# Kernel tuning notes

Hardware: AMD Instinct MI355X
Metric: run time of the kernel (lower is better)

The kernel has to match this reference:

```python
import jax, jax.numpy as jnp
import numpy as np

D_HEAD = 64
MASK_FILL = -1000000.0


def setup_inputs() -> dict:
    key = jax.random.key(0)
    ks = jax.random.split(key, 5)
    batch, seq, d_model, n_heads, d_head = 4, 2048, 1024, 16, D_HEAD
    # xavier_uniform bound for [d_model, n_heads, d_head]: treated as fan_in=d_model, fan_out=n_heads*d_head
    bound_qkv = float(np.sqrt(6.0 / (d_model + n_heads * d_head)))
    bound_out = float(np.sqrt(6.0 / (d_head + n_heads * d_model)))
    return {
        "resid": jax.random.normal(ks[0], (batch, seq, d_model), dtype=jnp.float32),
        "W_Q": jax.random.uniform(ks[1], (d_model, n_heads, d_head), jnp.float32, -bound_qkv, bound_qkv),
        "W_K": jax.random.uniform(ks[2], (d_model, n_heads, d_head), jnp.float32, -bound_qkv, bound_qkv),
        "W_V": jax.random.uniform(ks[3], (d_model, n_heads, d_head), jnp.float32, -bound_qkv, bound_qkv),
        "W_out": jax.random.uniform(ks[4], (d_head, n_heads, d_model), jnp.float32, -bound_out, bound_out),
        "b_out": jnp.zeros((d_model,), dtype=jnp.float32),
    }


def reference(resid, W_Q, W_K, W_V, W_out, b_out):
    # resid: [b, s, d]; W_Q/K/V: [d, h, dh]; W_out: [dh, h, d]
    seq = resid.shape[1]
    d_head = W_Q.shape[-1]
    q = jnp.einsum('bsd,dhk->bshk', resid, W_Q)
    k = jnp.einsum('bsd,dhk->bshk', resid, W_K)
    v = jnp.einsum('bsd,dhk->bshk', resid, W_V)
    scores = jnp.einsum('bqhk,bkhd->bhqd', q, k.astype(q.dtype)) if False else jnp.einsum('bqhc,bshc->bhqs', q, k)
    scores = scores / jnp.sqrt(jnp.asarray(d_head, dtype=scores.dtype))
    causal_mask = jnp.triu(jnp.ones((seq, seq), dtype=bool), k=1)
    scores = jnp.where(causal_mask, MASK_FILL, scores)
    probs = jax.nn.softmax(scores, axis=-1)  # [b, h, q, s]
    z = jnp.einsum('bhqs,bshc->bqhc', probs, v)
    out = jnp.einsum('bqhc,chd->bqd', z, W_out) + b_out
    return out
```

## Files before the change

kernel.cpp:

```cpp
#include <hip/hip_runtime.h>
#include <hip/hip_bf16.h>


typedef short s16x8 __attribute__((ext_vector_type(8)));
typedef short s16x4 __attribute__((ext_vector_type(4)));
typedef float f32x4 __attribute__((ext_vector_type(4)));

#define MFMA_BF16(A, B, C) __builtin_amdgcn_mfma_f32_16x16x32_bf16((A), (B), (C), 0, 0, 0)

#if __has_builtin(__builtin_amdgcn_exp2f)
#define EXP2(x) __builtin_amdgcn_exp2f(x)
#else
#define EXP2(x) exp2f(x)
#endif
#if __has_builtin(__builtin_amdgcn_rcpf)
#define RCP(x) __builtin_amdgcn_rcpf(x)
#else
#define RCP(x) (1.0f / (x))
#endif

__device__ __forceinline__ short f2bf(float f) {
    __bf16 h = (__bf16)f;
    return __builtin_bit_cast(short, h);
}

__device__ __forceinline__ void gld16(const unsigned short* g, unsigned short* l) {
    __builtin_amdgcn_global_load_lds(
        (const __attribute__((address_space(1))) unsigned int*)g,
        (__attribute__((address_space(3))) unsigned int*)l, 16, 0, 0);
}

__global__ __launch_bounds__(256) void prep_fused(
    const float* __restrict__ resid, const float* __restrict__ WQ,
    const float* __restrict__ WK, const float* __restrict__ WV,
    const float* __restrict__ Wout,
    unsigned short* __restrict__ residb, unsigned short* __restrict__ Wqkvt,
    unsigned short* __restrict__ W2t)
{
    const int bid = blockIdx.x;
    if (bid < 8192) {
        const int i = bid * 256 + threadIdx.x;
        const float4 v = ((const float4*)resid)[i];
        s16x4 o;
        o[0] = f2bf(v.x); o[1] = f2bf(v.y); o[2] = f2bf(v.z); o[3] = f2bf(v.w);
        *(s16x4*)(residb + (size_t)i * 4) = o;
        return;
    }
    __shared__ unsigned short tile[64][66];
    const int id2 = bid - 8192;
    const int which = id2 >> 8;
    const int sub = id2 & 255;
    const int tx = threadIdx.x & 63, ty = threadIdx.x >> 6;
    if (which < 3) {
        const float* W = which == 0 ? WQ : (which == 1 ? WK : WV);
        unsigned short* Wt = Wqkvt + (size_t)which * 1024 * 1024;
        const int n0 = (sub & 15) * 64, k0 = (sub >> 4) * 64;
        #pragma unroll
        for (int i = ty; i < 64; i += 4)
            tile[i][tx] = (unsigned short)f2bf(W[(size_t)(k0 + i) * 1024 + n0 + tx]);
        __syncthreads();
        #pragma unroll
        for (int i = ty; i < 64; i += 4)
            Wt[(size_t)(n0 + i) * 1024 + k0 + tx] = tile[tx][i];
    } else {
        const int d0 = (sub & 15) * 64, h = sub >> 4;
        #pragma unroll
        for (int c = ty; c < 64; c += 4)
            tile[c][tx] = (unsigned short)f2bf(Wout[(size_t)(c * 16 + h) * 1024 + d0 + tx]);
        __syncthreads();
        #pragma unroll
        for (int i = ty; i < 64; i += 4)
            W2t[(size_t)(d0 + i) * 1024 + h * 64 + tx] = tile[tx][i];
    }
}

__global__ __launch_bounds__(512, 2) void gemm_qkv(
    const unsigned short* __restrict__ A,
    const unsigned short* __restrict__ Bt,
    unsigned short* __restrict__ Qb, unsigned short* __restrict__ Kb,
    unsigned short* __restrict__ Vt)
{
    extern __shared__ __align__(16) unsigned short S[];
    constexpr int LDK = 1024, NT = 16;
    const int tid = threadIdx.x, lane = tid & 63, w = tid >> 6;
    const int wm = w >> 2, wn = w & 3;
    const int quad = lane >> 4, fl = lane & 15;

    const int wg  = blockIdx.x;
    const int swz = (wg & 7) * 96 + (wg >> 3);
    const int bx  = swz % 12, by = swz / 12;
    const int m0  = by * 128, n0 = bx * 256;

    const int srow = tid >> 2;
    const int sk   = ((tid & 3) ^ ((tid >> 3) & 3)) * 8;
    const unsigned short* pa  = A  + (size_t)(m0 + srow) * LDK + sk;
    const unsigned short* pb0 = Bt + (size_t)(n0 + srow) * LDK + sk;
    const unsigned short* pb1 = Bt + (size_t)(n0 + 128 + srow) * LDK + sk;
    const int dst = tid * 8;

    const int sx   = (quad ^ ((fl >> 1) & 3)) * 8;
    const int arow = (wm * 64 + fl) * 32 + sx;
    const int brow = 8192 + (wn * 64 + fl) * 32 + sx;

    f32x4 acc[4][4];
    #pragma unroll
    for (int m = 0; m < 4; ++m)
        #pragma unroll
        for (int n = 0; n < 4; ++n) acc[m][n] = (f32x4){0.f, 0.f, 0.f, 0.f};

    gld16(pa,       S + dst);
    gld16(pb0,      S + 8192 + dst);
    gld16(pb1,      S + 12288 + dst);
    gld16(pa + 32,  S + 4096 + dst);
    gld16(pb0 + 32, S + 16384 + dst);
    gld16(pb1 + 32, S + 20480 + dst);

    for (int t = 0; t < NT; ++t) {
        unsigned short* Sc = S + (t & 1) * 24576;
        unsigned short* Sn = S + ((t & 1) ^ 1) * 24576;
        const int ka = (t + 1) * 64;
        const bool pf = (t + 1 < NT);

        asm volatile("s_waitcnt vmcnt(3)" ::: "memory");
        __builtin_amdgcn_s_barrier();

        s16x8 af[4], bfr[4];
        #pragma unroll
        for (int mi = 0; mi < 4; ++mi) af[mi]  = *(const s16x8*)(Sc + arow + mi * 512);
        #pragma unroll
        for (int ni = 0; ni < 4; ++ni) bfr[ni] = *(const s16x8*)(Sc + brow + ni * 512);
        if (pf) {
            gld16(pa + ka,  Sn + dst);
            gld16(pb0 + ka, Sn + 8192 + dst);
            gld16(pb1 + ka, Sn + 12288 + dst);
        }
        asm volatile("" ::: "memory");
        __builtin_amdgcn_s_barrier();
        __builtin_amdgcn_s_setprio(1);
        #pragma unroll
        for (int mi = 0; mi < 4; ++mi)
            #pragma unroll
            for (int ni = 0; ni < 4; ++ni)
                acc[mi][ni] = MFMA_BF16(af[mi], bfr[ni], acc[mi][ni]);
        __builtin_amdgcn_s_setprio(0);

        if (pf) asm volatile("s_waitcnt vmcnt(3)" ::: "memory");
        else    asm volatile("s_waitcnt vmcnt(0)" ::: "memory");
        __builtin_amdgcn_s_barrier();
        #pragma unroll
        for (int mi = 0; mi < 4; ++mi) af[mi]  = *(const s16x8*)(Sc + 4096 + arow + mi * 512);
        #pragma unroll
        for (int ni = 0; ni < 4; ++ni) bfr[ni] = *(const s16x8*)(Sc + 8192 + brow + ni * 512);
        if (pf) {
            gld16(pa + ka + 32,  Sn + 4096 + dst);
            gld16(pb0 + ka + 32, Sn + 16384 + dst);
            gld16(pb1 + ka + 32, Sn + 20480 + dst);
        }
        asm volatile("" ::: "memory");
        __builtin_amdgcn_s_barrier();
        __builtin_amdgcn_s_setprio(1);
        #pragma unroll
        for (int mi = 0; mi < 4; ++mi)
            #pragma unroll
            for (int ni = 0; ni < 4; ++ni)
                acc[mi][ni] = MFMA_BF16(af[mi], bfr[ni], acc[mi][ni]);
        __builtin_amdgcn_s_setprio(0);
    }

    const int which = n0 >> 10;
    if (which < 2) {
        unsigned short* O = which == 0 ? Qb : Kb;
        const int cbase = (n0 & 1023) + wn * 64;
        #pragma unroll
        for (int mi = 0; mi < 4; ++mi) {
            const int row = m0 + wm * 64 + mi * 16 + quad * 4;
            #pragma unroll
            for (int ni = 0; ni < 4; ++ni) {
                const int col = cbase + ni * 16 + fl;
                #pragma unroll
                for (int r = 0; r < 4; ++r)
                    O[(size_t)(row + r) * 1024 + col] = (unsigned short)f2bf(acc[mi][ni][r]);
            }
        }
    } else {
        const int hh = ((n0 - 2048) >> 6) + wn;
        #pragma unroll
        for (int mi = 0; mi < 4; ++mi) {
            const int token = m0 + wm * 64 + mi * 16 + quad * 4;
            const int bb = token >> 11, ss = token & 2047;
            #pragma unroll
            for (int ni = 0; ni < 4; ++ni) {
                const int cl = ni * 16 + fl;
                s16x4 pv;
                pv[0] = f2bf(acc[mi][ni][0]); pv[1] = f2bf(acc[mi][ni][1]);
                pv[2] = f2bf(acc[mi][ni][2]); pv[3] = f2bf(acc[mi][ni][3]);
                *(s16x4*)(Vt + (size_t)((bb * 16 + hh) * 64 + cl) * 2048 + ss) = pv;
            }
        }
    }
}

template <int MODE>
__global__ __launch_bounds__(256, 2) void gemm_bt(
    const unsigned short* __restrict__ A,
    const unsigned short* __restrict__ Bt,
    float* __restrict__ Cf, const float* __restrict__ bias,
    int M, int N, int K)
{
    __shared__ __align__(16) unsigned short AB[2 * 128 * 72];
    const int tid  = threadIdx.x;
    const int lane = tid & 63;
    const int w    = tid >> 6;
    const int wm   = w & 1, wn = w >> 1;
    const int quad = lane >> 4, fl = lane & 15;
    const int m0 = blockIdx.y * 128, n0 = blockIdx.x * 128;

    const unsigned short* gp[9];
    unsigned ldso[9];
    #pragma unroll
    for (int i = 0; i < 9; ++i) {
        const int c = i * 256 + tid;
        const int cm = c % 1152;
        const int r = cm / 9, cl0 = cm % 9;
        const int cl = (cl0 == 8) ? 0 : cl0;
        gp[i] = (c < 1152 ? A + (size_t)(m0 + r) * K : Bt + (size_t)(n0 + r) * K) + cl * 8;
        ldso[i] = (unsigned)c * 8u;
    }

    f32x4 acc[4][4];
    #pragma unroll
    for (int i = 0; i < 4; ++i)
        #pragma unroll
        for (int j = 0; j < 4; ++j)
            acc[i][j] = (f32x4){0.f, 0.f, 0.f, 0.f};

    for (int kt = 0; kt < K; kt += 64) {
        __syncthreads();
        #pragma unroll
        for (int i = 0; i < 9; ++i)
            gld16(gp[i] + kt, AB + ldso[i]);
        __syncthreads();
        #pragma unroll
        for (int ko = 0; ko < 2; ++ko) {
            s16x8 af[4], bf[4];
            #pragma unroll
            for (int mi = 0; mi < 4; ++mi)
                af[mi] = *(const s16x8*)(AB + (wm * 64 + mi * 16 + fl) * 72 + ko * 32 + quad * 8);
            #pragma unroll
            for (int ni = 0; ni < 4; ++ni)
                bf[ni] = *(const s16x8*)(AB + 9216 + (wn * 64 + ni * 16 + fl) * 72 + ko * 32 + quad * 8);
            #pragma unroll
            for (int mi = 0; mi < 4; ++mi)
                #pragma unroll
                for (int ni = 0; ni < 4; ++ni)
                    acc[mi][ni] = MFMA_BF16(af[mi], bf[ni], acc[mi][ni]);
        }
    }

    #pragma unroll
    for (int ni = 0; ni < 4; ++ni) {
        const int col = n0 + wn * 64 + ni * 16 + fl;
        const float bv = bias[col];
        #pragma unroll
        for (int mi = 0; mi < 4; ++mi) {
            const int row = m0 + wm * 64 + mi * 16 + quad * 4;
            #pragma unroll
            for (int r = 0; r < 4; ++r)
                Cf[(size_t)(row + r) * N + col] = acc[mi][ni][r] + bv;
        }
    }
}

template <bool DIAG>
__device__ __forceinline__ void attn_tile(
    int s0, int wl, int wq0, int fl, int quad,
    const unsigned short* __restrict__ KV, const unsigned short* __restrict__ Vs,
    unsigned short* __restrict__ PbW,
    const s16x8 (&qfr)[2][2], f32x4 (&zt)[2][4], float (&ls)[2])
{
    const float SC = 0.18033688011112042f;
    const float M  = 32.0f;
    #pragma unroll
    for (int c4 = 0; c4 < 4; ++c4) {
        if (DIAG && c4 > wl) break;
        #pragma unroll
        for (int e = 0; e < 2; ++e) {
            const int f = 2 * c4 + e;
            const unsigned short* Krow = KV + (f * 16 + fl) * 72;
            const s16x8 kf0 = *(const s16x8*)(Krow + quad * 8);
            const s16x8 kf1 = *(const s16x8*)(Krow + 32 + quad * 8);
            #pragma unroll
            for (int g = 0; g < 2; ++g) {
                unsigned short* pw = PbW + (g * 16 + fl) * 36 + e * 16 + quad * 4;
                if (DIAG && f > 2 * wl + g) {
                    *(s16x4*)pw = (s16x4){0, 0, 0, 0};
                } else {
                    f32x4 z = (f32x4){0.f, 0.f, 0.f, 0.f};
                    z = MFMA_BF16(kf0, qfr[g][0], z);
                    z = MFMA_BF16(kf1, qfr[g][1], z);
                    float p[4];
                    #pragma unroll
                    for (int r = 0; r < 4; ++r) {
                        float arg = fmaf(z[r], SC, -M);
                        if (DIAG && f == 2 * wl + g) {
                            const int s = s0 + f * 16 + quad * 4 + r;
                            const int qi = wq0 + g * 16 + fl;
                            if (s > qi) arg = -100.f;
                        }
                        p[r] = EXP2(arg);
                    }
                    ls[g] += (p[0] + p[1]) + (p[2] + p[3]);
                    s16x4 pk;
                    pk[0] = f2bf(p[0]); pk[1] = f2bf(p[1]);
                    pk[2] = f2bf(p[2]); pk[3] = f2bf(p[3]);
                    *(s16x4*)pw = pk;
                }
            }
        }
        const s16x8 pf0 = *(const s16x8*)(PbW + fl * 36 + quad * 8);
        const s16x8 pf1 = *(const s16x8*)(PbW + (16 + fl) * 36 + quad * 8);
        #pragma unroll
        for (int mf = 0; mf < 4; ++mf) {
            const s16x8 vf = *(const s16x8*)(Vs + (mf * 16 + fl) * 136 + c4 * 32 + quad * 8);
            zt[0][mf] = MFMA_BF16(vf, pf0, zt[0][mf]);
            zt[1][mf] = MFMA_BF16(vf, pf1, zt[1][mf]);
        }
    }
}

__global__ __launch_bounds__(512, 4) void attn_causal(
    const unsigned short* __restrict__ Qb,
    const unsigned short* __restrict__ Kb,
    const unsigned short* __restrict__ Vt,
    unsigned short* __restrict__ Zb)
{
    __shared__ __align__(16) unsigned short KV[17920];
    __shared__ __align__(16) unsigned short Pb[8][32 * 36];
    const int tid = threadIdx.x, lane = tid & 63, w = tid >> 6;
    const int quad = lane >> 4, fl = lane & 15;
    const int lid = blockIdx.x;
    const int g8 = lid >> 6;
    const int qb = g8 < 4 ? 7 - g8 : g8 - 4;
    const int bh = lid & 63, b = bh >> 4, h = bh & 15;
    const int wq0 = qb * 256 + w * 32;
    const int wl = w & 3;
    const int dt = 2 * qb + (w >> 2);

    const unsigned short* Kbase = Kb + (size_t)b * 2048 * 1024 + h * 64;
    const unsigned short* Vbase = Vt + (size_t)bh * 64 * 2048;
    unsigned short* PbW = Pb[w];
    const unsigned short* Vs = KV + 9216;

    s16x8 qfr[2][2];
    #pragma unroll
    for (int g = 0; g < 2; ++g) {
        const unsigned short* Qrow = Qb + (size_t)(b * 2048 + wq0 + g * 16 + fl) * 1024 + h * 64;
        qfr[g][0] = *(const s16x8*)(Qrow + quad * 8);
        qfr[g][1] = *(const s16x8*)(Qrow + 32 + quad * 8);
    }

    const unsigned short* gsp[5];
    int sadv[5];
    unsigned ldsb[5];
    #pragma unroll
    for (int i = 0; i < 5; ++i) {
        const int W = w + 8 * i;
        if (W < 35) {
            const int c = W * 64 + lane;
            if (c < 1152) {
                const int r = c / 9, cl0 = c % 9;
                const int cl = (cl0 == 8) ? 0 : cl0;
                gsp[i] = Kbase + r * 1024 + cl * 8;  sadv[i] = 128 * 1024;
            } else {
                const int cc = c - 1152;
                const int r = cc / 17, cl0 = cc % 17;
                const int cl = (cl0 == 16) ? 0 : cl0;
                gsp[i] = Vbase + r * 2048 + cl * 8;  sadv[i] = 128;
            }
            ldsb[i] = (unsigned)c * 8u;
        }
    }

    f32x4 zt[2][4];
    #pragma unroll
    for (int g = 0; g < 2; ++g)
        #pragma unroll
        for (int mf = 0; mf < 4; ++mf) zt[g][mf] = (f32x4){0.f, 0.f, 0.f, 0.f};
    float ls[2] = {0.f, 0.f};
    const int ntiles = 2 * qb + 2;

    for (int kt = 0; kt < ntiles; ++kt) {
        __syncthreads();
        #pragma unroll
        for (int i = 0; i < 5; ++i)
            if (w + 8 * i < 35)
                gld16(gsp[i], KV + ldsb[i]);
        #pragma unroll
        for (int i = 0; i < 5; ++i)
            if (w + 8 * i < 35)
                gsp[i] += sadv[i];
        __syncthreads();

        if (kt < dt) {
            attn_tile<false>(kt << 7, wl, wq0, fl, quad, KV, Vs, PbW, qfr, zt, ls);
        } else if (kt == dt) {
            attn_tile<true>(kt << 7, wl, wq0, fl, quad, KV, Vs, PbW, qfr, zt, ls);
        }
    }
    #pragma unroll
    for (int g = 0; g < 2; ++g) {
        float lt = ls[g];
        lt += __shfl_xor(lt, 16);
        lt += __shfl_xor(lt, 32);
        const float inv = RCP(lt);
        unsigned short* Zrow = Zb + (size_t)(b * 2048 + wq0 + g * 16 + fl) * 1024 + h * 64;
        #pragma unroll
        for (int mf = 0; mf < 4; ++mf) {
            s16x4 o;
            o[0] = f2bf(zt[g][mf][0] * inv); o[1] = f2bf(zt[g][mf][1] * inv);
            o[2] = f2bf(zt[g][mf][2] * inv); o[3] = f2bf(zt[g][mf][3] * inv);
            *(s16x4*)(Zrow + mf * 16 + quad * 4) = o;
        }
    }
}

extern "C" void kernel_launch(void* const* d_in, const int* in_sizes, int n_in,
                              void* d_out, int out_size, void* d_ws, size_t ws_size,
                              hipStream_t stream) {
    const float* resid = (const float*)d_in[0];
    const float* WQ    = (const float*)d_in[1];
    const float* WK    = (const float*)d_in[2];
    const float* WV    = (const float*)d_in[3];
    const float* Wout  = (const float*)d_in[4];
    const float* bout  = (const float*)d_in[5];
    float* out = (float*)d_out;

    char* p = (char*)d_ws;
    auto alloc = [&](size_t bytes) { void* r = (void*)p; p += (bytes + 255) & ~(size_t)255; return r; };
    unsigned short* residb = (unsigned short*)alloc(8192ull * 1024 * 2);
    unsigned short* Wqkvt  = (unsigned short*)alloc(3072ull * 1024 * 2);
    unsigned short* W2t    = (unsigned short*)alloc(1024ull * 1024 * 2);
    unsigned short* Qbuf   = (unsigned short*)alloc(8192ull * 1024 * 2);
    unsigned short* Kbuf   = (unsigned short*)alloc(8192ull * 1024 * 2);
    unsigned short* Vtb    = (unsigned short*)alloc(64ull * 64 * 2048 * 2);
    unsigned short* Zbuf   = (unsigned short*)alloc(8192ull * 1024 * 2);

    static bool s_attr = false;
    if (!s_attr) {
        hipFuncSetAttribute(reinterpret_cast<const void*>(gemm_qkv),
                            hipFuncAttributeMaxDynamicSharedMemorySize, 98304);
        s_attr = true;
    }

    prep_fused<<<9216, 256, 0, stream>>>(resid, WQ, WK, WV, Wout, residb, Wqkvt, W2t);
    gemm_qkv<<<768, 512, 98304, stream>>>(residb, Wqkvt, Qbuf, Kbuf, Vtb);
    attn_causal<<<512, 512, 0, stream>>>(Qbuf, Kbuf, Vtb, Zbuf);
    gemm_bt<0><<<dim3(8, 64), 256, 0, stream>>>(Zbuf, W2t, out, bout, 8192, 1024, 1024);
}
```

Measured before the change: 263.5 us.

## Deepen QKV GEMM prefetch pipeline and shrink attention blocks to 128 queries

The QKV GEMM now prefetches half-tiles one stage further ahead, so three half-tile loads are in flight (vmcnt 6) instead of one, hiding more global-load latency. The attention kernel goes from 512-thread blocks covering 256 queries to 256-thread blocks covering 128 queries, launching 1024 blocks in longest-first order. Smaller blocks should improve load balance across the causal workload and avoid warps sitting idle on fully masked tiles. The cost is more K/V tile loading per query, since each block loads its own K/V, and more loads issued per thread.

```diff
diff --git a/kernel.cpp b/kernel.cpp
--- a/kernel.cpp
+++ b/kernel.cpp
@@ -114,14 +114,16 @@
     gld16(pa + 32,  S + 4096 + dst);
     gld16(pb0 + 32, S + 16384 + dst);
     gld16(pb1 + 32, S + 20480 + dst);
+    gld16(pa + 64,  S + 24576 + dst);
+    gld16(pb0 + 64, S + 24576 + 8192 + dst);
+    gld16(pb1 + 64, S + 24576 + 12288 + dst);
 
     for (int t = 0; t < NT; ++t) {
         unsigned short* Sc = S + (t & 1) * 24576;
         unsigned short* Sn = S + ((t & 1) ^ 1) * 24576;
-        const int ka = (t + 1) * 64;
-        const bool pf = (t + 1 < NT);
-
-        asm volatile("s_waitcnt vmcnt(3)" ::: "memory");
+
+        if (t < NT - 1) asm volatile("s_waitcnt vmcnt(6)" ::: "memory");
+        else            asm volatile("s_waitcnt vmcnt(3)" ::: "memory");
         __builtin_amdgcn_s_barrier();
 
         s16x8 af[4], bfr[4];
@@ -129,10 +131,11 @@
         for (int mi = 0; mi < 4; ++mi) af[mi]  = *(const s16x8*)(Sc + arow + mi * 512);
         #pragma unroll
         for (int ni = 0; ni < 4; ++ni) bfr[ni] = *(const s16x8*)(Sc + brow + ni * 512);
-        if (pf) {
-            gld16(pa + ka,  Sn + dst);
-            gld16(pb0 + ka, Sn + 8192 + dst);
-            gld16(pb1 + ka, Sn + 12288 + dst);
+        if (t < NT - 1) {
+            const int ka = (t + 1) * 64 + 32;
+            gld16(pa + ka,  Sn + 4096 + dst);
+            gld16(pb0 + ka, Sn + 16384 + dst);
+            gld16(pb1 + ka, Sn + 20480 + dst);
         }
         asm volatile("" ::: "memory");
         __builtin_amdgcn_s_barrier();
@@ -144,17 +147,18 @@
                 acc[mi][ni] = MFMA_BF16(af[mi], bfr[ni], acc[mi][ni]);
         __builtin_amdgcn_s_setprio(0);
 
-        if (pf) asm volatile("s_waitcnt vmcnt(3)" ::: "memory");
-        else    asm volatile("s_waitcnt vmcnt(0)" ::: "memory");
+        if (t < NT - 1) asm volatile("s_waitcnt vmcnt(6)" ::: "memory");
+        else            asm volatile("s_waitcnt vmcnt(0)" ::: "memory");
         __builtin_amdgcn_s_barrier();
         #pragma unroll
         for (int mi = 0; mi < 4; ++mi) af[mi]  = *(const s16x8*)(Sc + 4096 + arow + mi * 512);
         #pragma unroll
         for (int ni = 0; ni < 4; ++ni) bfr[ni] = *(const s16x8*)(Sc + 8192 + brow + ni * 512);
-        if (pf) {
-            gld16(pa + ka + 32,  Sn + 4096 + dst);
-            gld16(pb0 + ka + 32, Sn + 16384 + dst);
-            gld16(pb1 + ka + 32, Sn + 20480 + dst);
+        if (t < NT - 2) {
+            const int ka = (t + 2) * 64;
+            gld16(pa + ka,  Sc + dst);
+            gld16(pb0 + ka, Sc + 8192 + dst);
+            gld16(pb1 + ka, Sc + 12288 + dst);
         }
         asm volatile("" ::: "memory");
         __builtin_amdgcn_s_barrier();
@@ -328,23 +332,21 @@
     }
 }
 
-__global__ __launch_bounds__(512, 4) void attn_causal(
+__global__ __launch_bounds__(256, 3) void attn_causal(
     const unsigned short* __restrict__ Qb,
     const unsigned short* __restrict__ Kb,
     const unsigned short* __restrict__ Vt,
     unsigned short* __restrict__ Zb)
 {
     __shared__ __align__(16) unsigned short KV[17920];
-    __shared__ __align__(16) unsigned short Pb[8][32 * 36];
+    __shared__ __align__(16) unsigned short Pb[4][32 * 36];
     const int tid = threadIdx.x, lane = tid & 63, w = tid >> 6;
     const int quad = lane >> 4, fl = lane & 15;
     const int lid = blockIdx.x;
-    const int g8 = lid >> 6;
-    const int qb = g8 < 4 ? 7 - g8 : g8 - 4;
+    const int qb = 15 - (lid >> 6);
     const int bh = lid & 63, b = bh >> 4, h = bh & 15;
-    const int wq0 = qb * 256 + w * 32;
-    const int wl = w & 3;
-    const int dt = 2 * qb + (w >> 2);
+    const int wq0 = qb * 128 + w * 32;
+    const int wl = w;
 
     const unsigned short* Kbase = Kb + (size_t)b * 2048 * 1024 + h * 64;
     const unsigned short* Vbase = Vt + (size_t)bh * 64 * 2048;
@@ -359,12 +361,12 @@
         qfr[g][1] = *(const s16x8*)(Qrow + 32 + quad * 8);
     }
 
-    const unsigned short* gsp[5];
-    int sadv[5];
-    unsigned ldsb[5];
-    #pragma unroll
-    for (int i = 0; i < 5; ++i) {
-        const int W = w + 8 * i;
+    const unsigned short* gsp[9];
+    int sadv[9];
+    unsigned ldsb[9];
+    #pragma unroll
+    for (int i = 0; i < 9; ++i) {
+        const int W = w + 4 * i;
         if (W < 35) {
             const int c = W * 64 + lane;
             if (c < 1152) {
@@ -387,23 +389,23 @@
         #pragma unroll
         for (int mf = 0; mf < 4; ++mf) zt[g][mf] = (f32x4){0.f, 0.f, 0.f, 0.f};
     float ls[2] = {0.f, 0.f};
-    const int ntiles = 2 * qb + 2;
+    const int ntiles = qb + 1;
 
     for (int kt = 0; kt < ntiles; ++kt) {
         __syncthreads();
         #pragma unroll
-        for (int i = 0; i < 5; ++i)
-            if (w + 8 * i < 35)
+        for (int i = 0; i < 9; ++i)
+            if (w + 4 * i < 35)
                 gld16(gsp[i], KV + ldsb[i]);
         #pragma unroll
-        for (int i = 0; i < 5; ++i)
-            if (w + 8 * i < 35)
+        for (int i = 0; i < 9; ++i)
+            if (w + 4 * i < 35)
                 gsp[i] += sadv[i];
         __syncthreads();
 
-        if (kt < dt) {
+        if (kt < qb) {
             attn_tile<false>(kt << 7, wl, wq0, fl, quad, KV, Vs, PbW, qfr, zt, ls);
-        } else if (kt == dt) {
+        } else {
             attn_tile<true>(kt << 7, wl, wq0, fl, quad, KV, Vs, PbW, qfr, zt, ls);
         }
     }
@@ -454,6 +456,6 @@
 
     prep_fused<<<9216, 256, 0, stream>>>(resid, WQ, WK, WV, Wout, residb, Wqkvt, W2t);
     gemm_qkv<<<768, 512, 98304, stream>>>(residb, Wqkvt, Qbuf, Kbuf, Vtb);
-    attn_causal<<<512, 512, 0, stream>>>(Qbuf, Kbuf, Vtb, Zbuf);
+    attn_causal<<<1024, 256, 0, stream>>>(Qbuf, Kbuf, Vtb, Zbuf);
     gemm_bt<0><<<dim3(8, 64), 256, 0, stream>>>(Zbuf, W2t, out, bout, 8192, 1024, 1024);
 }
```

Result: no change. 265.4 us (+0.7%).
